# Kernel tuning notes

Measured on AMD Instinct MI355X. Metric: run time of the kernel, lower is better.

## Reference

```python
import jax, jax.numpy as jnp
import numpy as np
from jax import lax

T = 5        # unrolled ISTA iterations (module default)
LAM = 0.1    # soft-threshold level (module default)
B, L, K = 4096, 4096, 128


def _conv1d_same(x, k):
    """TF-style SAME cross-correlation. x: [B, L], k: [K] -> [B, L]."""
    Kw = k.shape[0]
    pad_left = (Kw - 1) // 2
    pad_right = Kw - 1 - pad_left
    out = lax.conv_general_dilated(
        x[:, None, :],            # [B, 1, L]
        k[None, None, :],         # [O=1, I=1, K]
        window_strides=(1,),
        padding=[(pad_left, pad_right)],
        dimension_numbers=("NCH", "OIH", "NCH"),
    )
    return out[:, 0, :]


def setup_inputs() -> dict:
    key = jax.random.key(0)
    k1, k2 = jax.random.split(key)
    y = jax.random.normal(k1, (B, L), dtype=jnp.float32)
    thz_pulse = jax.random.normal(k2, (K,), dtype=jnp.float32)  # learned pulse (trainable)
    step_size = jnp.full((1,), 0.1, dtype=jnp.float32)          # learned step (trainable)
    return {"y": y, "thz_pulse": thz_pulse, "step_size": step_size}


def reference(y, thz_pulse, step_size):
    x = jnp.zeros_like(y)
    h = thz_pulse           # matched-filter kernel
    h_rev = thz_pulse[::-1] # time-reversed kernel (adjoint / correlation)
    s = step_size[0]
    for _ in range(T):
        conv_out = _conv1d_same(y, h)           # H y
        residual = y - conv_out                 # y - H y
        update = _conv1d_same(residual, h_rev)  # H^T residual
        x = x + s * update                      # gradient step
        x = jnp.sign(x) * jax.nn.relu(jnp.abs(x) - LAM)  # soft-threshold
    return x
```

## Files before the change

kernel.cpp:

```cpp
#include <hip/hip_runtime.h>


typedef __bf16 bf16;
typedef __bf16 bf16x4 __attribute__((ext_vector_type(4)));
typedef __bf16 bf16x8 __attribute__((ext_vector_type(8)));
typedef float f32x4 __attribute__((ext_vector_type(4)));

#define LC 512
#define PY 792
#define LAM 0.1f

__global__ __launch_bounds__(256) void ista_g(
    const float* __restrict__ y, const float* __restrict__ h,
    const float* __restrict__ step, float* __restrict__ out) {
  __shared__ __align__(16) bf16 ys[16 * PY];
  __shared__ __align__(16) bf16 gpad[384];
  __shared__ float hs[256];

  const int tid = threadIdx.x;
  const int lane = tid & 63;
  const int li = lane & 15;
  const int quad = lane >> 4;
  const int wave = tid >> 6;
  const int bid = blockIdx.x;
  const int chunk0 = (bid >> 8) * LC;
  const int b0 = (bid & 255) * 16;

  {
    float hv = 0.f;
    if (tid < 128) hv = h[tid];
    hs[tid] = hv;
  }

  {
    const int rr = tid >> 4;
    const int t = tid & 15;
    const float* yrow = y + (size_t)(b0 + rr) * 4096;
    bf16* dst = ys + rr * PY;
#pragma unroll
    for (int k = 0; k < 13; ++k) {
      int s4 = t + 16 * k;
      if (s4 < 196) {
        int l = chunk0 - 128 + s4 * 4;
        float4 v;
        if (l >= 0 && l <= 4096 - 4) {
          v = *reinterpret_cast<const float4*>(yrow + l);
        } else {
          v.x = ((unsigned)(l + 0) < 4096u) ? yrow[l + 0] : 0.f;
          v.y = ((unsigned)(l + 1) < 4096u) ? yrow[l + 1] : 0.f;
          v.z = ((unsigned)(l + 2) < 4096u) ? yrow[l + 2] : 0.f;
          v.w = ((unsigned)(l + 3) < 4096u) ? yrow[l + 3] : 0.f;
        }
        bf16x4 bv;
        bv[0] = (bf16)v.x; bv[1] = (bf16)v.y; bv[2] = (bf16)v.z; bv[3] = (bf16)v.w;
        *reinterpret_cast<bf16x4*>(dst + s4 * 4) = bv;
      }
    }
  }
  __syncthreads();

  if (tid < 128) {
    const int tau = tid;
    float ac = 0.f;
#pragma unroll 8
    for (int m = 0; m < 128; ++m) ac += hs[m] * hs[m + tau];
    float g1 = (tau <= 63) ? hs[63 - tau] : 0.f;
    gpad[145 + tau] = (bf16)(g1 - ac);
    if (tau > 0) {
      float g2 = (tau <= 64) ? hs[63 + tau] : 0.f;
      gpad[145 - tau] = (bf16)(g2 - ac);
    }
  } else {
    const int r = tid - 128;
    if (r < 18) gpad[r] = (bf16)0.f;
    if (273 + r < 384) gpad[273 + r] = (bf16)0.f;
  }
  __syncthreads();

  bf16x8 AG[9];
  {
    const int off = 144 + quad * 8 - li;
#pragma unroll
    for (int dd = 0; dd < 9; ++dd) {
      bf16x8 a;
      const int o = off + (dd - 4) * 32;
#pragma unroll
      for (int j = 0; j < 8; ++j) a[j] = gpad[o + j];
      AG[dd] = a;
    }
  }

  const float s = step[0];
  for (int t = wave; t < 32; t += 4) {
    const int i0 = 16 * t;
    f32x4 acc0 = {0.f, 0.f, 0.f, 0.f};
    f32x4 acc1 = {0.f, 0.f, 0.f, 0.f};
    const bf16* brow = ys + li * PY + (i0 + 128) + quad * 8;
#pragma unroll
    for (int dd = 0; dd < 9; dd += 2) {
      bf16x8 b = *reinterpret_cast<const bf16x8*>(brow + (dd - 4) * 32);
      acc0 = __builtin_amdgcn_mfma_f32_16x16x32_bf16(AG[dd], b, acc0, 0, 0, 0);
    }
#pragma unroll
    for (int dd = 1; dd < 9; dd += 2) {
      bf16x8 b = *reinterpret_cast<const bf16x8*>(brow + (dd - 4) * 32);
      acc1 = __builtin_amdgcn_mfma_f32_16x16x32_bf16(AG[dd], b, acc1, 0, 0, 0);
    }
    float4 xv;
#pragma unroll
    for (int e = 0; e < 4; ++e) {
      float su = s * (acc0[e] + acc1[e]);
      float ax = fabsf(su) - LAM;
      ax = ax > 0.f ? ax : 0.f;
      (&xv.x)[e] = 5.f * copysignf(ax, su);
    }
    *reinterpret_cast<float4*>(
        out + (size_t)(b0 + li) * 4096 + chunk0 + i0 + quad * 4) = xv;
  }
}

#define EC 64
#define PYE 360
#define PRE 216
__global__ __launch_bounds__(256) void ista_edge(
    const float* __restrict__ y, const float* __restrict__ h,
    const float* __restrict__ step, float* __restrict__ out) {
  __shared__ __align__(16) bf16 ys[16 * PYE];
  __shared__ __align__(16) bf16 rs[16 * PRE];
  __shared__ __align__(16) bf16 h1p[256], h2p[256];

  const int tid = threadIdx.x;
  const int lane = tid & 63;
  const int li = lane & 15;
  const int quad = lane >> 4;
  const int wave = tid >> 6;
  const int bid = blockIdx.x;
  const int chunk0 = (bid & 1) ? (4096 - EC) : 0;
  const int b0 = (bid >> 1) * 16;

  {
    const int p = tid;
    int i1 = p - 64;
    h1p[p] = ((unsigned)i1 < 128u) ? (bf16)h[i1] : (bf16)0.f;
    int i2 = 191 - p;
    h2p[p] = ((unsigned)i2 < 128u) ? (bf16)(-h[i2]) : (bf16)0.f;
  }

  {
    const int rr = tid >> 4;
    const int t = tid & 15;
    const float* yrow = y + (size_t)(b0 + rr) * 4096;
    bf16* dst = ys + rr * PYE;
#pragma unroll
    for (int k = 0; k < 6; ++k) {
      int s4 = t + 16 * k;
      if (s4 < 88) {
        int l = chunk0 - 128 + s4 * 4;
        float4 v;
        if (l >= 0 && l <= 4096 - 4) {
          v = *reinterpret_cast<const float4*>(yrow + l);
        } else {
          v.x = ((unsigned)(l + 0) < 4096u) ? yrow[l + 0] : 0.f;
          v.y = ((unsigned)(l + 1) < 4096u) ? yrow[l + 1] : 0.f;
          v.z = ((unsigned)(l + 2) < 4096u) ? yrow[l + 2] : 0.f;
          v.w = ((unsigned)(l + 3) < 4096u) ? yrow[l + 3] : 0.f;
        }
        bf16x4 bv;
        bv[0] = (bf16)v.x; bv[1] = (bf16)v.y; bv[2] = (bf16)v.z; bv[3] = (bf16)v.w;
        *reinterpret_cast<bf16x4*>(dst + s4 * 4) = bv;
      }
    }
  }
  __syncthreads();

  bf16x8 A1[5], A2[5];
  {
    const int off = 127 + quad * 8 - li;
#pragma unroll
    for (int dd = 0; dd < 5; ++dd) {
      const int o = off + (dd - 2) * 32;
      bf16x8 a1, a2;
#pragma unroll
      for (int j = 0; j < 8; ++j) { a1[j] = h1p[o + j]; a2[j] = h2p[o + j]; }
      A1[dd] = a1; A2[dd] = a2;
    }
  }

  for (int t = wave; t < 13; t += 4) {
    const int i0 = -64 + 16 * t;
    f32x4 acc;
    {
      bf16x4 yv = *reinterpret_cast<const bf16x4*>(
          ys + li * PYE + (i0 + 128) + quad * 4);
      acc[0] = -(float)yv[0]; acc[1] = -(float)yv[1];
      acc[2] = -(float)yv[2]; acc[3] = -(float)yv[3];
    }
#pragma unroll
    for (int dd = 0; dd < 5; ++dd) {
      bf16x8 b = *reinterpret_cast<const bf16x8*>(
          ys + li * PYE + (i0 + (dd - 2) * 32 + 128) + quad * 8);
      acc = __builtin_amdgcn_mfma_f32_16x16x32_bf16(A1[dd], b, acc, 0, 0, 0);
    }
    bf16x4 rv;
#pragma unroll
    for (int e = 0; e < 4; ++e) {
      int g = chunk0 + i0 + quad * 4 + e;
      float v = ((unsigned)g < 4096u) ? acc[e] : 0.f;
      rv[e] = (bf16)v;
    }
    *reinterpret_cast<bf16x4*>(rs + li * PRE + (i0 + 64) + quad * 4) = rv;
  }
  __syncthreads();

  const float s = step[0];
  for (int t = wave; t < 4; t += 4) {
    const int i0 = 16 * t;
    f32x4 acc = {0.f, 0.f, 0.f, 0.f};
#pragma unroll
    for (int dd = 0; dd < 5; ++dd) {
      bf16x8 b = *reinterpret_cast<const bf16x8*>(
          rs + li * PRE + (i0 + (dd - 2) * 32 + 64) + quad * 8);
      acc = __builtin_amdgcn_mfma_f32_16x16x32_bf16(A2[dd], b, acc, 0, 0, 0);
    }
    float4 xv;
#pragma unroll
    for (int e = 0; e < 4; ++e) {
      float su = s * acc[e];
      float ax = fabsf(su) - LAM;
      ax = ax > 0.f ? ax : 0.f;
      (&xv.x)[e] = 5.f * copysignf(ax, su);
    }
    *reinterpret_cast<float4*>(
        out + (size_t)(b0 + li) * 4096 + chunk0 + i0 + quad * 4) = xv;
  }
}

extern "C" void kernel_launch(void* const* d_in, const int* in_sizes, int n_in,
                              void* d_out, int out_size, void* d_ws,
                              size_t ws_size, hipStream_t stream) {
  const float* y = (const float*)d_in[0];
  const float* h = (const float*)d_in[1];
  const float* s = (const float*)d_in[2];
  float* out = (float*)d_out;
  ista_g<<<dim3(8 * 256), dim3(256), 0, stream>>>(y, h, s, out);
  ista_edge<<<dim3(2 * 256), dim3(256), 0, stream>>>(y, h, s, out);
}
```

Baseline: 149.3 us.

## Precompute filter fragments once and fuse interior and edge kernels

A one-block prep kernel now computes the composite filter (autocorrelation plus the reversed pulse) and the MFMA A-fragments once, writing them to workspace. Previously every block recomputed a 128-term autocorrelation in shared memory. The interior and edge kernels are merged into a single launch, and interior blocks no longer write the edge columns that the edge path recomputes. The interior inner loop keeps a sliding register window of B fragments, and interior chunks take a fast load path with no bounds checks. The cost is an extra tiny serial launch before the main kernel and higher register pressure from holding B[9].

```diff
diff --git a/kernel.cpp b/kernel.cpp
--- a/kernel.cpp
+++ b/kernel.cpp
@@ -7,231 +7,261 @@
 typedef float f32x4 __attribute__((ext_vector_type(4)));
 
 #define LC 512
-#define PY 792
+#define PY 824
 #define LAM 0.1f
-
-__global__ __launch_bounds__(256) void ista_g(
-    const float* __restrict__ y, const float* __restrict__ h,
+#define WS_AG 0
+#define WS_A1 8192
+#define WS_A2 12288
+#define PYE 360
+#define PRE 216
+
+__global__ __launch_bounds__(256) void ista_prep(const float* __restrict__ h,
+                                                 bf16* __restrict__ ws) {
+  __shared__ float hs[256];
+  __shared__ float acp[256];
+  __shared__ bf16 gp[384];
+  const int tid = threadIdx.x;
+  hs[tid] = (tid < 128) ? h[tid] : 0.f;
+  gp[tid] = (bf16)0.f;
+  if (tid < 128) gp[256 + tid] = (bf16)0.f;
+  __syncthreads();
+  const int tau = tid & 127;
+  {
+    const int m0 = (tid >> 7) * 64;
+    float p0 = 0.f, p1 = 0.f, p2 = 0.f, p3 = 0.f;
+    for (int m = m0; m < m0 + 64; m += 4) {
+      p0 += hs[m] * hs[m + tau];     p1 += hs[m + 1] * hs[m + 1 + tau];
+      p2 += hs[m + 2] * hs[m + 2 + tau]; p3 += hs[m + 3] * hs[m + 3 + tau];
+    }
+    acp[tid] = (p0 + p1) + (p2 + p3);
+  }
+  __syncthreads();
+  if (tid < 128) {
+    float ac = acp[tid] + acp[tid + 128];
+    float g1 = (tau <= 63) ? hs[63 - tau] : 0.f;
+    gp[145 + tau] = (bf16)(g1 - ac);
+    if (tau > 0) {
+      float g2 = (tau <= 64) ? hs[63 + tau] : 0.f;
+      gp[145 - tau] = (bf16)(g2 - ac);
+    }
+  }
+  __syncthreads();
+  for (int i = tid; i < 1024; i += 256) {
+    const int l = i >> 4, dd = i & 15;
+    if (dd < 9) {
+      const int o = 144 + (l >> 4) * 8 - (l & 15) + (dd - 4) * 32;
+      bf16x8 a;
+#pragma unroll
+      for (int j = 0; j < 8; ++j) a[j] = gp[o + j];
+      *reinterpret_cast<bf16x8*>(ws + WS_AG + l * 128 + dd * 8) = a;
+    }
+  }
+  for (int i = tid; i < 512; i += 256) {
+    const int l = i >> 3, dd = i & 7;
+    if (dd < 5) {
+      const int o = 127 + (l >> 4) * 8 - (l & 15) + (dd - 2) * 32;
+      bf16x8 a1, a2;
+#pragma unroll
+      for (int j = 0; j < 8; ++j) {
+        int p = o + j;
+        int i1 = p - 64;
+        a1[j] = ((unsigned)i1 < 128u) ? (bf16)hs[i1] : (bf16)0.f;
+        int i2 = 191 - p;
+        a2[j] = ((unsigned)i2 < 128u) ? (bf16)(-hs[i2]) : (bf16)0.f;
+      }
+      *reinterpret_cast<bf16x8*>(ws + WS_A1 + l * 64 + dd * 8) = a1;
+      *reinterpret_cast<bf16x8*>(ws + WS_A2 + l * 64 + dd * 8) = a2;
+    }
+  }
+}
+
+__global__ __launch_bounds__(256) void ista_fused(
+    const float* __restrict__ y, const bf16* __restrict__ ws,
     const float* __restrict__ step, float* __restrict__ out) {
-  __shared__ __align__(16) bf16 ys[16 * PY];
-  __shared__ __align__(16) bf16 gpad[384];
-  __shared__ float hs[256];
-
+  __shared__ __align__(16) bf16 buf[16 * PY];
   const int tid = threadIdx.x;
   const int lane = tid & 63;
   const int li = lane & 15;
   const int quad = lane >> 4;
   const int wave = tid >> 6;
   const int bid = blockIdx.x;
-  const int chunk0 = (bid >> 8) * LC;
-  const int b0 = (bid & 255) * 16;
-
-  {
-    float hv = 0.f;
-    if (tid < 128) hv = h[tid];
-    hs[tid] = hv;
-  }
-
-  {
-    const int rr = tid >> 4;
-    const int t = tid & 15;
-    const float* yrow = y + (size_t)(b0 + rr) * 4096;
-    bf16* dst = ys + rr * PY;
-#pragma unroll
-    for (int k = 0; k < 13; ++k) {
-      int s4 = t + 16 * k;
-      if (s4 < 196) {
-        int l = chunk0 - 128 + s4 * 4;
-        float4 v;
-        if (l >= 0 && l <= 4096 - 4) {
-          v = *reinterpret_cast<const float4*>(yrow + l);
-        } else {
-          v.x = ((unsigned)(l + 0) < 4096u) ? yrow[l + 0] : 0.f;
-          v.y = ((unsigned)(l + 1) < 4096u) ? yrow[l + 1] : 0.f;
-          v.z = ((unsigned)(l + 2) < 4096u) ? yrow[l + 2] : 0.f;
-          v.w = ((unsigned)(l + 3) < 4096u) ? yrow[l + 3] : 0.f;
-        }
-        bf16x4 bv;
-        bv[0] = (bf16)v.x; bv[1] = (bf16)v.y; bv[2] = (bf16)v.z; bv[3] = (bf16)v.w;
-        *reinterpret_cast<bf16x4*>(dst + s4 * 4) = bv;
-      }
-    }
-  }
-  __syncthreads();
-
-  if (tid < 128) {
-    const int tau = tid;
-    float ac = 0.f;
-#pragma unroll 8
-    for (int m = 0; m < 128; ++m) ac += hs[m] * hs[m + tau];
-    float g1 = (tau <= 63) ? hs[63 - tau] : 0.f;
-    gpad[145 + tau] = (bf16)(g1 - ac);
-    if (tau > 0) {
-      float g2 = (tau <= 64) ? hs[63 + tau] : 0.f;
-      gpad[145 - tau] = (bf16)(g2 - ac);
+  const float s = step[0];
+
+  if (bid < 2048) {
+    const int chunk0 = (bid >> 8) * LC;
+    const int b0 = (bid & 255) * 16;
+
+    bf16x8 AG[9];
+#pragma unroll
+    for (int dd = 0; dd < 9; ++dd)
+      AG[dd] = *reinterpret_cast<const bf16x8*>(ws + WS_AG + lane * 128 + dd * 8);
+
+    {
+      const int rr = tid >> 4;
+      const int t = tid & 15;
+      const float* yrow = y + (size_t)(b0 + rr) * 4096;
+      bf16* dst = buf + rr * PY;
+      if (chunk0 != 0 && chunk0 != 3584) {
+#pragma unroll
+        for (int k = 0; k < 13; ++k) {
+          int s4 = t + 16 * k;
+          if (s4 < 200) {
+            float4 v = *reinterpret_cast<const float4*>(yrow + chunk0 - 128 + s4 * 4);
+            bf16x4 bv;
+            bv[0] = (bf16)v.x; bv[1] = (bf16)v.y; bv[2] = (bf16)v.z; bv[3] = (bf16)v.w;
+            *reinterpret_cast<bf16x4*>(dst + s4 * 4) = bv;
+          }
+        }
+      } else {
+#pragma unroll
+        for (int k = 0; k < 13; ++k) {
+          int s4 = t + 16 * k;
+          if (s4 < 200) {
+            int l = chunk0 - 128 + s4 * 4;
+            float4 v;
+            if (l >= 0 && l <= 4096 - 4) {
+              v = *reinterpret_cast<const float4*>(yrow + l);
+            } else {
+              v.x = ((unsigned)(l + 0) < 4096u) ? yrow[l + 0] : 0.f;
+              v.y = ((unsigned)(l + 1) < 4096u) ? yrow[l + 1] : 0.f;
+              v.z = ((unsigned)(l + 2) < 4096u) ? yrow[l + 2] : 0.f;
+              v.w = ((unsigned)(l + 3) < 4096u) ? yrow[l + 3] : 0.f;
+            }
+            bf16x4 bv;
+            bv[0] = (bf16)v.x; bv[1] = (bf16)v.y; bv[2] = (bf16)v.z; bv[3] = (bf16)v.w;
+            *reinterpret_cast<bf16x4*>(dst + s4 * 4) = bv;
+          }
+        }
+      }
+    }
+    __syncthreads();
+
+    const bf16* brow = buf + li * PY + 128 + quad * 8;
+    const int iw = 16 * wave;
+    bf16x8 B[9];
+#pragma unroll
+    for (int dd = 0; dd < 9; ++dd)
+      B[dd] = *reinterpret_cast<const bf16x8*>(brow + iw + (dd - 4) * 32);
+    float* orow = out + (size_t)(b0 + li) * 4096 + chunk0 + iw + quad * 4;
+#pragma unroll
+    for (int k = 0; k < 8; ++k) {
+      f32x4 acc0 = {0.f, 0.f, 0.f, 0.f};
+      f32x4 acc1 = {0.f, 0.f, 0.f, 0.f};
+      acc0 = __builtin_amdgcn_mfma_f32_16x16x32_bf16(AG[0], B[0], acc0, 0, 0, 0);
+      acc1 = __builtin_amdgcn_mfma_f32_16x16x32_bf16(AG[1], B[1], acc1, 0, 0, 0);
+      acc0 = __builtin_amdgcn_mfma_f32_16x16x32_bf16(AG[2], B[2], acc0, 0, 0, 0);
+      acc1 = __builtin_amdgcn_mfma_f32_16x16x32_bf16(AG[3], B[3], acc1, 0, 0, 0);
+      acc0 = __builtin_amdgcn_mfma_f32_16x16x32_bf16(AG[4], B[4], acc0, 0, 0, 0);
+      acc1 = __builtin_amdgcn_mfma_f32_16x16x32_bf16(AG[5], B[5], acc1, 0, 0, 0);
+      acc0 = __builtin_amdgcn_mfma_f32_16x16x32_bf16(AG[6], B[6], acc0, 0, 0, 0);
+      acc1 = __builtin_amdgcn_mfma_f32_16x16x32_bf16(AG[7], B[7], acc1, 0, 0, 0);
+      acc0 = __builtin_amdgcn_mfma_f32_16x16x32_bf16(AG[8], B[8], acc0, 0, 0, 0);
+      const int gc0 = chunk0 + iw + 64 * k;
+      if (gc0 >= 64 && gc0 < 4032) {
+        float4 xv;
+#pragma unroll
+        for (int e = 0; e < 4; ++e) {
+          float su = s * (acc0[e] + acc1[e]);
+          float ax = fabsf(su) - LAM;
+          ax = ax > 0.f ? ax : 0.f;
+          (&xv.x)[e] = 5.f * copysignf(ax, su);
+        }
+        *reinterpret_cast<float4*>(orow + 64 * k) = xv;
+      }
+      if (k < 7) {
+#pragma unroll
+        for (int r = 0; r < 7; ++r) B[r] = B[r + 2];
+        B[7] = *reinterpret_cast<const bf16x8*>(brow + iw + 64 * (k + 1) + 96);
+        B[8] = *reinterpret_cast<const bf16x8*>(brow + iw + 64 * (k + 1) + 128);
+      }
     }
   } else {
-    const int r = tid - 128;
-    if (r < 18) gpad[r] = (bf16)0.f;
-    if (273 + r < 384) gpad[273 + r] = (bf16)0.f;
-  }
-  __syncthreads();
-
-  bf16x8 AG[9];
-  {
-    const int off = 144 + quad * 8 - li;
-#pragma unroll
-    for (int dd = 0; dd < 9; ++dd) {
-      bf16x8 a;
-      const int o = off + (dd - 4) * 32;
-#pragma unroll
-      for (int j = 0; j < 8; ++j) a[j] = gpad[o + j];
-      AG[dd] = a;
-    }
-  }
-
-  const float s = step[0];
-  for (int t = wave; t < 32; t += 4) {
-    const int i0 = 16 * t;
-    f32x4 acc0 = {0.f, 0.f, 0.f, 0.f};
-    f32x4 acc1 = {0.f, 0.f, 0.f, 0.f};
-    const bf16* brow = ys + li * PY + (i0 + 128) + quad * 8;
-#pragma unroll
-    for (int dd = 0; dd < 9; dd += 2) {
-      bf16x8 b = *reinterpret_cast<const bf16x8*>(brow + (dd - 4) * 32);
-      acc0 = __builtin_amdgcn_mfma_f32_16x16x32_bf16(AG[dd], b, acc0, 0, 0, 0);
-    }
-#pragma unroll
-    for (int dd = 1; dd < 9; dd += 2) {
-      bf16x8 b = *reinterpret_cast<const bf16x8*>(brow + (dd - 4) * 32);
-      acc1 = __builtin_amdgcn_mfma_f32_16x16x32_bf16(AG[dd], b, acc1, 0, 0, 0);
-    }
-    float4 xv;
-#pragma unroll
-    for (int e = 0; e < 4; ++e) {
-      float su = s * (acc0[e] + acc1[e]);
-      float ax = fabsf(su) - LAM;
-      ax = ax > 0.f ? ax : 0.f;
-      (&xv.x)[e] = 5.f * copysignf(ax, su);
-    }
-    *reinterpret_cast<float4*>(
-        out + (size_t)(b0 + li) * 4096 + chunk0 + i0 + quad * 4) = xv;
-  }
-}
-
-#define EC 64
-#define PYE 360
-#define PRE 216
-__global__ __launch_bounds__(256) void ista_edge(
-    const float* __restrict__ y, const float* __restrict__ h,
-    const float* __restrict__ step, float* __restrict__ out) {
-  __shared__ __align__(16) bf16 ys[16 * PYE];
-  __shared__ __align__(16) bf16 rs[16 * PRE];
-  __shared__ __align__(16) bf16 h1p[256], h2p[256];
-
-  const int tid = threadIdx.x;
-  const int lane = tid & 63;
-  const int li = lane & 15;
-  const int quad = lane >> 4;
-  const int wave = tid >> 6;
-  const int bid = blockIdx.x;
-  const int chunk0 = (bid & 1) ? (4096 - EC) : 0;
-  const int b0 = (bid >> 1) * 16;
-
-  {
-    const int p = tid;
-    int i1 = p - 64;
-    h1p[p] = ((unsigned)i1 < 128u) ? (bf16)h[i1] : (bf16)0.f;
-    int i2 = 191 - p;
-    h2p[p] = ((unsigned)i2 < 128u) ? (bf16)(-h[i2]) : (bf16)0.f;
-  }
-
-  {
-    const int rr = tid >> 4;
-    const int t = tid & 15;
-    const float* yrow = y + (size_t)(b0 + rr) * 4096;
-    bf16* dst = ys + rr * PYE;
-#pragma unroll
-    for (int k = 0; k < 6; ++k) {
-      int s4 = t + 16 * k;
-      if (s4 < 88) {
-        int l = chunk0 - 128 + s4 * 4;
-        float4 v;
-        if (l >= 0 && l <= 4096 - 4) {
-          v = *reinterpret_cast<const float4*>(yrow + l);
-        } else {
-          v.x = ((unsigned)(l + 0) < 4096u) ? yrow[l + 0] : 0.f;
-          v.y = ((unsigned)(l + 1) < 4096u) ? yrow[l + 1] : 0.f;
-          v.z = ((unsigned)(l + 2) < 4096u) ? yrow[l + 2] : 0.f;
-          v.w = ((unsigned)(l + 3) < 4096u) ? yrow[l + 3] : 0.f;
-        }
-        bf16x4 bv;
-        bv[0] = (bf16)v.x; bv[1] = (bf16)v.y; bv[2] = (bf16)v.z; bv[3] = (bf16)v.w;
-        *reinterpret_cast<bf16x4*>(dst + s4 * 4) = bv;
-      }
-    }
-  }
-  __syncthreads();
-
-  bf16x8 A1[5], A2[5];
-  {
-    const int off = 127 + quad * 8 - li;
+    const int eid = bid - 2048;
+    const int chunk0 = (eid & 1) ? (4096 - 64) : 0;
+    const int b0 = (eid >> 1) * 16;
+    bf16* ys = buf;
+    bf16* rs = buf + 16 * PYE;
+
+    bf16x8 A1[5], A2[5];
 #pragma unroll
     for (int dd = 0; dd < 5; ++dd) {
-      const int o = off + (dd - 2) * 32;
-      bf16x8 a1, a2;
-#pragma unroll
-      for (int j = 0; j < 8; ++j) { a1[j] = h1p[o + j]; a2[j] = h2p[o + j]; }
-      A1[dd] = a1; A2[dd] = a2;
-    }
-  }
-
-  for (int t = wave; t < 13; t += 4) {
-    const int i0 = -64 + 16 * t;
-    f32x4 acc;
+      A1[dd] = *reinterpret_cast<const bf16x8*>(ws + WS_A1 + lane * 64 + dd * 8);
+      A2[dd] = *reinterpret_cast<const bf16x8*>(ws + WS_A2 + lane * 64 + dd * 8);
+    }
+
     {
-      bf16x4 yv = *reinterpret_cast<const bf16x4*>(
-          ys + li * PYE + (i0 + 128) + quad * 4);
-      acc[0] = -(float)yv[0]; acc[1] = -(float)yv[1];
-      acc[2] = -(float)yv[2]; acc[3] = -(float)yv[3];
-    }
-#pragma unroll
-    for (int dd = 0; dd < 5; ++dd) {
-      bf16x8 b = *reinterpret_cast<const bf16x8*>(
-          ys + li * PYE + (i0 + (dd - 2) * 32 + 128) + quad * 8);
-      acc = __builtin_amdgcn_mfma_f32_16x16x32_bf16(A1[dd], b, acc, 0, 0, 0);
-    }
-    bf16x4 rv;
-#pragma unroll
-    for (int e = 0; e < 4; ++e) {
-      int g = chunk0 + i0 + quad * 4 + e;
-      float v = ((unsigned)g < 4096u) ? acc[e] : 0.f;
-      rv[e] = (bf16)v;
-    }
-    *reinterpret_cast<bf16x4*>(rs + li * PRE + (i0 + 64) + quad * 4) = rv;
-  }
-  __syncthreads();
-
-  const float s = step[0];
-  for (int t = wave; t < 4; t += 4) {
-    const int i0 = 16 * t;
-    f32x4 acc = {0.f, 0.f, 0.f, 0.f};
-#pragma unroll
-    for (int dd = 0; dd < 5; ++dd) {
-      bf16x8 b = *reinterpret_cast<const bf16x8*>(
-          rs + li * PRE + (i0 + (dd - 2) * 32 + 64) + quad * 8);
-      acc = __builtin_amdgcn_mfma_f32_16x16x32_bf16(A2[dd], b, acc, 0, 0, 0);
-    }
-    float4 xv;
-#pragma unroll
-    for (int e = 0; e < 4; ++e) {
-      float su = s * acc[e];
-      float ax = fabsf(su) - LAM;
-      ax = ax > 0.f ? ax : 0.f;
-      (&xv.x)[e] = 5.f * copysignf(ax, su);
-    }
-    *reinterpret_cast<float4*>(
-        out + (size_t)(b0 + li) * 4096 + chunk0 + i0 + quad * 4) = xv;
+      const int rr = tid >> 4;
+      const int t = tid & 15;
+      const float* yrow = y + (size_t)(b0 + rr) * 4096;
+      bf16* dst = ys + rr * PYE;
+#pragma unroll
+      for (int k = 0; k < 6; ++k) {
+        int s4 = t + 16 * k;
+        if (s4 < 88) {
+          int l = chunk0 - 128 + s4 * 4;
+          float4 v;
+          if (l >= 0 && l <= 4096 - 4) {
+            v = *reinterpret_cast<const float4*>(yrow + l);
+          } else {
+            v.x = ((unsigned)(l + 0) < 4096u) ? yrow[l + 0] : 0.f;
+            v.y = ((unsigned)(l + 1) < 4096u) ? yrow[l + 1] : 0.f;
+            v.z = ((unsigned)(l + 2) < 4096u) ? yrow[l + 2] : 0.f;
+            v.w = ((unsigned)(l + 3) < 4096u) ? yrow[l + 3] : 0.f;
+          }
+          bf16x4 bv;
+          bv[0] = (bf16)v.x; bv[1] = (bf16)v.y; bv[2] = (bf16)v.z; bv[3] = (bf16)v.w;
+          *reinterpret_cast<bf16x4*>(dst + s4 * 4) = bv;
+        }
+      }
+    }
+    __syncthreads();
+
+    for (int t = wave; t < 13; t += 4) {
+      const int i0 = -64 + 16 * t;
+      f32x4 acc;
+      {
+        bf16x4 yv = *reinterpret_cast<const bf16x4*>(
+            ys + li * PYE + (i0 + 128) + quad * 4);
+        acc[0] = -(float)yv[0]; acc[1] = -(float)yv[1];
+        acc[2] = -(float)yv[2]; acc[3] = -(float)yv[3];
+      }
+#pragma unroll
+      for (int dd = 0; dd < 5; ++dd) {
+        bf16x8 b = *reinterpret_cast<const bf16x8*>(
+            ys + li * PYE + (i0 + (dd - 2) * 32 + 128) + quad * 8);
+        acc = __builtin_amdgcn_mfma_f32_16x16x32_bf16(A1[dd], b, acc, 0, 0, 0);
+      }
+      bf16x4 rv;
+#pragma unroll
+      for (int e = 0; e < 4; ++e) {
+        int g = chunk0 + i0 + quad * 4 + e;
+        float v = ((unsigned)g < 4096u) ? acc[e] : 0.f;
+        rv[e] = (bf16)v;
+      }
+      *reinterpret_cast<bf16x4*>(rs + li * PRE + (i0 + 64) + quad * 4) = rv;
+    }
+    __syncthreads();
+
+    {
+      const int i0 = 16 * wave;
+      f32x4 acc = {0.f, 0.f, 0.f, 0.f};
+#pragma unroll
+      for (int dd = 0; dd < 5; ++dd) {
+        bf16x8 b = *reinterpret_cast<const bf16x8*>(
+            rs + li * PRE + (i0 + (dd - 2) * 32 + 64) + quad * 8);
+        acc = __builtin_amdgcn_mfma_f32_16x16x32_bf16(A2[dd], b, acc, 0, 0, 0);
+      }
+      float4 xv;
+#pragma unroll
+      for (int e = 0; e < 4; ++e) {
+        float su = s * acc[e];
+        float ax = fabsf(su) - LAM;
+        ax = ax > 0.f ? ax : 0.f;
+        (&xv.x)[e] = 5.f * copysignf(ax, su);
+      }
+      *reinterpret_cast<float4*>(
+          out + (size_t)(b0 + li) * 4096 + chunk0 + i0 + quad * 4) = xv;
+    }
   }
 }
 
@@ -242,6 +272,7 @@
   const float* h = (const float*)d_in[1];
   const float* s = (const float*)d_in[2];
   float* out = (float*)d_out;
-  ista_g<<<dim3(8 * 256), dim3(256), 0, stream>>>(y, h, s, out);
-  ista_edge<<<dim3(2 * 256), dim3(256), 0, stream>>>(y, h, s, out);
+  bf16* ws = (bf16*)d_ws;
+  ista_prep<<<dim3(1), dim3(256), 0, stream>>>(h, ws);
+  ista_fused<<<dim3(2048 + 512), dim3(256), 0, stream>>>(y, ws, s, out);
 }
```

Measured after the change: 133.1 us. 1.12x faster.
